# Kernel tuning notes

Hardware: AMD Instinct MI355X
Metric: run time of the kernel (lower is better)

## Reference

```python
import jax, jax.numpy as jnp
import numpy as np

B, S, DIM, H = 2, 4096, 512, 8
HD = DIM // H
SCALE = HD ** -0.5
EPS = 1e-5


def setup_inputs() -> dict:
    key = jax.random.key(0)
    ks = jax.random.split(key, 7)
    std = DIM ** -0.5
    return {
        "x": jax.random.normal(ks[0], (B, S, DIM), dtype=jnp.float32),
        "ln_gamma": jnp.ones((DIM,), jnp.float32),
        "ln_beta": jnp.zeros((DIM,), jnp.float32),
        "w_q": jax.random.normal(ks[1], (DIM, DIM), jnp.float32) * std,
        "w_k": jax.random.normal(ks[2], (DIM, DIM), jnp.float32) * std,
        "w_v": jax.random.normal(ks[3], (DIM, DIM), jnp.float32) * std,
        "w_fc": jax.random.normal(ks[4], (DIM, DIM), jnp.float32) * std,
    }


def reference(x, ln_gamma, ln_beta, w_q, w_k, w_v, w_fc):
    # LayerNorm over last dim
    mu = jnp.mean(x, axis=-1, keepdims=True)
    var = jnp.var(x, axis=-1, keepdims=True)
    xn = (x - mu) * jax.lax.rsqrt(var + EPS) * ln_gamma + ln_beta
    # QKV projections (torch Linear: y = x @ W.T), split into heads -> [B,H,S,HD]
    q = jnp.einsum('bsd,ed->bse', xn, w_q).reshape(B, S, H, HD).transpose(0, 2, 1, 3)
    k = jnp.einsum('bsd,ed->bse', xn, w_k).reshape(B, S, H, HD).transpose(0, 2, 1, 3)
    v = jnp.einsum('bsd,ed->bse', xn, w_v).reshape(B, S, H, HD).transpose(0, 2, 1, 3)
    # scores [B,H,S,S]
    attn = jnp.einsum('bhqd,bhkd->bhqk', q, k) * SCALE
    attn = jax.nn.softmax(attn, axis=-1)
    # dropout is identity in eval mode
    out = jnp.einsum('bhqk,bhkd->bhqd', attn, v)
    out = out.transpose(0, 2, 1, 3).reshape(B, S, DIM)
    return jnp.einsum('bsd,ed->bse', out, w_fc)
```

## Files before the change

### kernel.cpp

```cpp
#include <hip/hip_runtime.h>
#include <cstdint>
#include <cstddef>

typedef unsigned short u16;
typedef unsigned int   u32;
typedef __bf16 bf16x8 __attribute__((ext_vector_type(8)));
typedef float  f32x4  __attribute__((ext_vector_type(4)));
typedef float  f32x16 __attribute__((ext_vector_type(16)));
typedef u16    u16x8  __attribute__((ext_vector_type(8)));
typedef u16    u16x4  __attribute__((ext_vector_type(4)));
typedef u32    u32x2  __attribute__((ext_vector_type(2)));
typedef u32    u32x4  __attribute__((ext_vector_type(4)));

#define DI __device__ __forceinline__

constexpr int SEQ = 4096;
constexpr int DIM = 512;
constexpr int NH  = 8;
constexpr int HD  = 64;
constexpr float ATT_C1 = 0.125f * 1.44269504088896340736f;

DI u16 f2bf(float f) {
  u32 u = __builtin_bit_cast(u32, f);
  u += 0x7fffu + ((u >> 16) & 1u);
  return (u16)(u >> 16);
}

DI u32 pk2(float hi, float lo) {
  u32 uh = __builtin_bit_cast(u32, hi) + 0x8000u;
  u32 ul = __builtin_bit_cast(u32, lo) + 0x8000u;
  return __builtin_amdgcn_perm(uh, ul, 0x07060302u);
}

__global__ __launch_bounds__(256) void wconv_kernel(
    const float* __restrict__ wq, const float* __restrict__ wk,
    const float* __restrict__ wv, const float* __restrict__ wfc,
    u16* __restrict__ Wb)
{
  const int idx  = blockIdx.x * 256 + threadIdx.x;
  const int base = idx * 8;
  const int mat  = base >> 18;
  const int off  = base & (512 * 512 - 1);
  const float* src = (mat == 0) ? wq : (mat == 1) ? wk : (mat == 2) ? wv : wfc;
  const float4 a = *(const float4*)(src + off);
  const float4 b = *(const float4*)(src + off + 4);
  u32x4 o = { pk2(a.y, a.x), pk2(a.w, a.z), pk2(b.y, b.x), pk2(b.w, b.z) };
  *(u32x4*)(Wb + base) = o;
}

__global__ __launch_bounds__(256) void ln_cast_kernel(
    const float* __restrict__ x, const float* __restrict__ gamma,
    const float* __restrict__ beta, u16* __restrict__ xn)
{
  const int row  = blockIdx.x * 4 + (threadIdx.x >> 6);
  const int lane = threadIdx.x & 63;
  const float* xr = x + (size_t)row * DIM + lane * 8;
  const float4 a = *(const float4*)xr;
  const float4 b = *(const float4*)(xr + 4);
  float s = a.x + a.y + a.z + a.w + b.x + b.y + b.z + b.w;
  float q = a.x*a.x + a.y*a.y + a.z*a.z + a.w*a.w
          + b.x*b.x + b.y*b.y + b.z*b.z + b.w*b.w;
#pragma unroll
  for (int m = 1; m < 64; m <<= 1) {
    s += __shfl_xor(s, m, 64);
    q += __shfl_xor(q, m, 64);
  }
  const float mu = s * (1.0f / DIM);
  const float rs = rsqrtf(q * (1.0f / DIM) - mu * mu + 1e-5f);
  const float4 g0 = *(const float4*)(gamma + lane * 8);
  const float4 g1 = *(const float4*)(gamma + lane * 8 + 4);
  const float4 e0 = *(const float4*)(beta + lane * 8);
  const float4 e1 = *(const float4*)(beta + lane * 8 + 4);
  const float v0 = (a.x - mu) * rs * g0.x + e0.x;
  const float v1 = (a.y - mu) * rs * g0.y + e0.y;
  const float v2 = (a.z - mu) * rs * g0.z + e0.z;
  const float v3 = (a.w - mu) * rs * g0.w + e0.w;
  const float v4 = (b.x - mu) * rs * g1.x + e1.x;
  const float v5 = (b.y - mu) * rs * g1.y + e1.y;
  const float v6 = (b.z - mu) * rs * g1.z + e1.z;
  const float v7 = (b.w - mu) * rs * g1.w + e1.w;
  u32x4 o = { pk2(v1, v0), pk2(v3, v2), pk2(v5, v4), pk2(v7, v6) };
  *(u32x4*)(xn + (size_t)row * DIM + lane * 8) = o;
}

template<int MODE>
__global__ __launch_bounds__(256, 2) void gemm_kernel(
    const u16* __restrict__ A, const u16* __restrict__ Wb,
    u16* __restrict__ Qo, u16* __restrict__ Ko, u16* __restrict__ Vt,
    float* __restrict__ Co)
{
  __shared__ u16 As[128][72];
  __shared__ u16 Bs[128][72];
  const int m0 = blockIdx.y * 128, n0 = blockIdx.x * 128;
  const int t = threadIdx.x, wave = t >> 6, lane = t & 63;
  const int quad = lane >> 4, l15 = lane & 15;
  const int wm = wave >> 1, wn = wave & 1;
  const u16* Wsrc;
  if (MODE == 0) {
    const int mat = n0 >> 9;
    Wsrc = Wb + (size_t)mat * 512 * 512 + (size_t)(n0 & 511) * DIM;
  } else {
    Wsrc = Wb + (size_t)3 * 512 * 512 + (size_t)n0 * DIM;
  }

  f32x4 acc[4][4];
#pragma unroll
  for (int i = 0; i < 4; i++)
#pragma unroll
    for (int j = 0; j < 4; j++)
#pragma unroll
      for (int r = 0; r < 4; r++) acc[i][j][r] = 0.0f;

  for (int kk = 0; kk < DIM; kk += 64) {
    __syncthreads();
#pragma unroll
    for (int it = 0; it < 4; it++) {
      const int c4 = t + it * 256;
      const int r = c4 >> 3, off = (c4 & 7) * 8;
      *(u16x8*)&As[r][off] =
          *(const u16x8*)(A + (size_t)(m0 + r) * DIM + kk + off);
      *(u16x8*)&Bs[r][off] =
          *(const u16x8*)(Wsrc + (size_t)r * DIM + kk + off);
    }
    __syncthreads();
#pragma unroll
    for (int kx = 0; kx < 2; kx++) {
      bf16x8 af[4], bfr[4];
#pragma unroll
      for (int i = 0; i < 4; i++)
        af[i] = *(const bf16x8*)&As[wm * 64 + i * 16 + l15][kx * 32 + quad * 8];
#pragma unroll
      for (int j = 0; j < 4; j++)
        bfr[j] = *(const bf16x8*)&Bs[wn * 64 + j * 16 + l15][kx * 32 + quad * 8];
#pragma unroll
      for (int i = 0; i < 4; i++)
#pragma unroll
        for (int j = 0; j < 4; j++)
          acc[i][j] = __builtin_amdgcn_mfma_f32_16x16x32_bf16(
              af[i], bfr[j], acc[i][j], 0, 0, 0);
    }
  }

  if (MODE == 1) {
#pragma unroll
    for (int i = 0; i < 4; i++) {
      const int m = m0 + wm * 64 + i * 16 + quad * 4;
#pragma unroll
      for (int j = 0; j < 4; j++) {
        const int n = n0 + wn * 64 + j * 16 + l15;
#pragma unroll
        for (int r = 0; r < 4; r++)
          Co[(size_t)(m + r) * DIM + n] = acc[i][j][r];
      }
    }
  } else {
    const int mat = n0 >> 9;
    const float qs = (mat == 0) ? ATT_C1 : 1.0f;
#pragma unroll
    for (int i = 0; i < 4; i++) {
      const int m = m0 + wm * 64 + i * 16 + quad * 4;
      const int b = m >> 12, s = m & 4095;
#pragma unroll
      for (int j = 0; j < 4; j++) {
        const int ng = (n0 & 511) + wn * 64 + j * 16 + l15;
        const int h = ng >> 6, d = ng & 63;
        if (mat < 2) {
          u16* dst = (mat == 0 ? Qo : Ko) +
                     ((size_t)(b * NH + h) * SEQ) * HD + d;
#pragma unroll
          for (int r = 0; r < 4; r++)
            dst[(size_t)(s + r) * HD] = f2bf(acc[i][j][r] * qs);
        } else {
          u32x2 w;
          w[0] = pk2(acc[i][j][1], acc[i][j][0]);
          w[1] = pk2(acc[i][j][3], acc[i][j][2]);
          *(u32x2*)&Vt[((size_t)(b * NH + h) * HD + d) * SEQ + s] = w;
        }
      }
    }
  }
}

__global__ __launch_bounds__(256, 2) void attn_kernel(
    const u16* __restrict__ Q, const u16* __restrict__ K,
    const u16* __restrict__ Vt, u16* __restrict__ O)
{
  __shared__ u16 Kl[128][72];
  __shared__ u16 Vl[64][136];
  __shared__ u16 Pl[4][32][136];
  const int qt = blockIdx.x, bh = blockIdx.y;
  const int b = bh >> 3, h = bh & 7;
  const int t = threadIdx.x, wave = t >> 6, lane = t & 63;
  const int l31 = lane & 31, hf = lane >> 5;
  const u16* Qb = Q + (size_t)bh * SEQ * HD;
  const u16* Kb = K + (size_t)bh * SEQ * HD;
  const u16* Vb = Vt + (size_t)bh * HD * SEQ;
  const int qw = qt * 128 + wave * 32;

  bf16x8 bq[4];
#pragma unroll
  for (int kk = 0; kk < 4; kk++)
    bq[kk] = *(const bf16x8*)(Qb + (size_t)(qw + l31) * HD + kk * 16 + hf * 8);

  f32x16 oacc[2];
#pragma unroll
  for (int mt = 0; mt < 2; mt++)
#pragma unroll
    for (int r = 0; r < 16; r++) oacc[mt][r] = 0.0f;
  float lrun = 0.0f;

  for (int kc = 0; kc < SEQ; kc += 128) {
    __syncthreads();
#pragma unroll
    for (int it = 0; it < 4; it++) {
      const int c4 = t + it * 256;
      {
        const int r = c4 >> 3, off = (c4 & 7) * 8;
        *(u16x8*)&Kl[r][off] =
            *(const u16x8*)(Kb + (size_t)(kc + r) * HD + off);
      }
      {
        const int d = c4 >> 4, off = (c4 & 15) * 8;
        *(u16x8*)&Vl[d][off] =
            *(const u16x8*)(Vb + (size_t)d * SEQ + kc + off);
      }
    }
    __syncthreads();

    f32x16 sacc[4];
#pragma unroll
    for (int mt = 0; mt < 4; mt++)
#pragma unroll
      for (int r = 0; r < 16; r++) sacc[mt][r] = 0.0f;
#pragma unroll
    for (int kk = 0; kk < 4; kk++) {
#pragma unroll
      for (int mt = 0; mt < 4; mt++) {
        const bf16x8 ka =
            *(const bf16x8*)&Kl[mt * 32 + l31][kk * 16 + hf * 8];
        sacc[mt] = __builtin_amdgcn_mfma_f32_32x32x16_bf16(
            ka, bq[kk], sacc[mt], 0, 0, 0);
      }
    }

    float ps = 0.0f;
#pragma unroll
    for (int mt = 0; mt < 4; mt++)
#pragma unroll
      for (int r = 0; r < 16; r++) {
        const float p = __builtin_amdgcn_exp2f(sacc[mt][r]);
        sacc[mt][r] = p;
        ps += p;
      }
    lrun += ps;

#pragma unroll
    for (int mt = 0; mt < 4; mt++)
#pragma unroll
      for (int g = 0; g < 4; g++) {
        u32x2 w;
        w[0] = pk2(sacc[mt][g * 4 + 1], sacc[mt][g * 4 + 0]);
        w[1] = pk2(sacc[mt][g * 4 + 3], sacc[mt][g * 4 + 2]);
        *(u32x2*)&Pl[wave][l31][mt * 32 + g * 8 + hf * 4] = w;
      }

#pragma unroll
    for (int kk2 = 0; kk2 < 8; kk2++) {
      const bf16x8 pb = *(const bf16x8*)&Pl[wave][l31][kk2 * 16 + hf * 8];
#pragma unroll
      for (int mt2 = 0; mt2 < 2; mt2++) {
        const bf16x8 va =
            *(const bf16x8*)&Vl[mt2 * 32 + l31][kk2 * 16 + hf * 8];
        oacc[mt2] = __builtin_amdgcn_mfma_f32_32x32x16_bf16(
            va, pb, oacc[mt2], 0, 0, 0);
      }
    }
  }

  const float lt = lrun + __shfl_xor(lrun, 32, 64);
  const float inv = 1.0f / lt;
  const int s = qw + l31;
  u16* Ob = O + ((size_t)(b * SEQ + s)) * DIM + h * HD;
#pragma unroll
  for (int mt2 = 0; mt2 < 2; mt2++)
#pragma unroll
    for (int g = 0; g < 4; g++) {
      u32x2 w;
      w[0] = pk2(oacc[mt2][g * 4 + 1] * inv, oacc[mt2][g * 4 + 0] * inv);
      w[1] = pk2(oacc[mt2][g * 4 + 3] * inv, oacc[mt2][g * 4 + 2] * inv);
      *(u32x2*)&Ob[mt2 * 32 + g * 8 + hf * 4] = w;
    }
}

extern "C" void kernel_launch(void* const* d_in, const int* in_sizes, int n_in,
                              void* d_out, int out_size, void* d_ws,
                              size_t ws_size, hipStream_t stream)
{
  const float* x     = (const float*)d_in[0];
  const float* gamma = (const float*)d_in[1];
  const float* beta  = (const float*)d_in[2];
  const float* wq    = (const float*)d_in[3];
  const float* wk    = (const float*)d_in[4];
  const float* wv    = (const float*)d_in[5];
  const float* wfc   = (const float*)d_in[6];
  float* out = (float*)d_out;

  char* ws = (char*)d_ws;
  u16* xn = (u16*)(ws);
  u16* Qb = (u16*)(ws + ((size_t)8  << 20));
  u16* Kb = (u16*)(ws + ((size_t)16 << 20));
  u16* Vt = (u16*)(ws + ((size_t)24 << 20));
  u16* Ob = (u16*)(ws + ((size_t)32 << 20));
  u16* Wb = (u16*)(ws + ((size_t)40 << 20));

  wconv_kernel<<<512, 256, 0, stream>>>(wq, wk, wv, wfc, Wb);
  ln_cast_kernel<<<2048, 256, 0, stream>>>(x, gamma, beta, xn);
  gemm_kernel<0><<<dim3(12, 64), 256, 0, stream>>>(xn, Wb, Qb, Kb, Vt, nullptr);
  attn_kernel<<<dim3(32, 16), 256, 0, stream>>>(Qb, Kb, Vt, Ob);
  gemm_kernel<1><<<dim3(4, 64), 256, 0, stream>>>(
      Ob, Wb, nullptr, nullptr, nullptr, out);
}
```

Measured before the change: 214.4 us.

## Keep P in registers via permlane swap, prefetch K/V to registers, remap blocks

The attention kernel no longer round-trips the softmax probabilities through LDS. It packs them with v_cvt_pk_bf16_f32 and rearranges them with v_permlane32_swap into the MFMA B-operand layout. Next-tile K/V loads are issued into registers before compute to overlap global latency, and QK^T, exp and PV are interleaved per 32-key subtile with s_setprio hints. Block indices are also remapped to interleave heads across CUs. This relies on gfx950-specific instructions and on the permlane swap exactly matching the MFMA layout, and it adds register pressure.

```diff
diff --git a/kernel.cpp b/kernel.cpp
--- a/kernel.cpp
+++ b/kernel.cpp
@@ -30,6 +30,16 @@
   u32 uh = __builtin_bit_cast(u32, hi) + 0x8000u;
   u32 ul = __builtin_bit_cast(u32, lo) + 0x8000u;
   return __builtin_amdgcn_perm(uh, ul, 0x07060302u);
+}
+
+DI u32 cvtpk(float a, float b) {
+  u32 r;
+  asm("v_cvt_pk_bf16_f32 %0, %1, %2" : "=v"(r) : "v"(a), "v"(b));
+  return r;
+}
+
+DI void plswap(u32& a, u32& b) {
+  asm("v_permlane32_swap_b32 %0, %1" : "+v"(a), "+v"(b));
 }
 
 __global__ __launch_bounds__(256) void wconv_kernel(
@@ -187,8 +197,10 @@
 {
   __shared__ u16 Kl[128][72];
   __shared__ u16 Vl[64][136];
-  __shared__ u16 Pl[4][32][136];
-  const int qt = blockIdx.x, bh = blockIdx.y;
+  const int flat = blockIdx.x + 32 * blockIdx.y;
+  const int slot = flat >> 3;
+  const int bh = (flat & 7) * 2 + (slot & 1);
+  const int qt = slot >> 1;
   const int b = bh >> 3, h = bh & 7;
   const int t = threadIdx.x, wave = t >> 6, lane = t & 63;
   const int l31 = lane & 31, hf = lane >> 5;
@@ -209,71 +221,87 @@
     for (int r = 0; r < 16; r++) oacc[mt][r] = 0.0f;
   float lrun = 0.0f;
 
+  const int st_r  = t >> 3,  st_off = (t & 7) * 8;
+  const int st_d  = t >> 4,  st_o2  = (t & 15) * 8;
+
+  u16x8 kst[4], vst[4];
+#pragma unroll
+  for (int it = 0; it < 4; it++) {
+    const int c4 = t + it * 256;
+    const int r = c4 >> 3, off = (c4 & 7) * 8;
+    kst[it] = *(const u16x8*)(Kb + (size_t)r * HD + off);
+    const int d = c4 >> 4, o2 = (c4 & 15) * 8;
+    vst[it] = *(const u16x8*)(Vb + (size_t)d * SEQ + o2);
+  }
+
   for (int kc = 0; kc < SEQ; kc += 128) {
     __syncthreads();
 #pragma unroll
     for (int it = 0; it < 4; it++) {
       const int c4 = t + it * 256;
-      {
+      const int r = c4 >> 3, off = (c4 & 7) * 8;
+      *(u16x8*)&Kl[r][off] = kst[it];
+      const int d = c4 >> 4, o2 = (c4 & 15) * 8;
+      *(u16x8*)&Vl[d][o2] = vst[it];
+    }
+    __syncthreads();
+    if (kc + 128 < SEQ) {
+#pragma unroll
+      for (int it = 0; it < 4; it++) {
+        const int c4 = t + it * 256;
         const int r = c4 >> 3, off = (c4 & 7) * 8;
-        *(u16x8*)&Kl[r][off] =
-            *(const u16x8*)(Kb + (size_t)(kc + r) * HD + off);
-      }
-      {
-        const int d = c4 >> 4, off = (c4 & 15) * 8;
-        *(u16x8*)&Vl[d][off] =
-            *(const u16x8*)(Vb + (size_t)d * SEQ + kc + off);
-      }
-    }
-    __syncthreads();
-
-    f32x16 sacc[4];
-#pragma unroll
-    for (int mt = 0; mt < 4; mt++)
-#pragma unroll
-      for (int r = 0; r < 16; r++) sacc[mt][r] = 0.0f;
-#pragma unroll
-    for (int kk = 0; kk < 4; kk++) {
-#pragma unroll
-      for (int mt = 0; mt < 4; mt++) {
+        kst[it] = *(const u16x8*)(Kb + (size_t)(kc + 128 + r) * HD + off);
+        const int d = c4 >> 4, o2 = (c4 & 15) * 8;
+        vst[it] = *(const u16x8*)(Vb + (size_t)d * SEQ + kc + 128 + o2);
+      }
+    }
+
+#pragma unroll
+    for (int mt = 0; mt < 4; mt++) {
+      f32x16 s;
+#pragma unroll
+      for (int r = 0; r < 16; r++) s[r] = 0.0f;
+      __builtin_amdgcn_s_setprio(1);
+#pragma unroll
+      for (int kk = 0; kk < 4; kk++) {
         const bf16x8 ka =
             *(const bf16x8*)&Kl[mt * 32 + l31][kk * 16 + hf * 8];
-        sacc[mt] = __builtin_amdgcn_mfma_f32_32x32x16_bf16(
-            ka, bq[kk], sacc[mt], 0, 0, 0);
-      }
-    }
-
-    float ps = 0.0f;
-#pragma unroll
-    for (int mt = 0; mt < 4; mt++)
-#pragma unroll
-      for (int r = 0; r < 16; r++) {
-        const float p = __builtin_amdgcn_exp2f(sacc[mt][r]);
-        sacc[mt][r] = p;
-        ps += p;
-      }
-    lrun += ps;
-
-#pragma unroll
-    for (int mt = 0; mt < 4; mt++)
-#pragma unroll
-      for (int g = 0; g < 4; g++) {
-        u32x2 w;
-        w[0] = pk2(sacc[mt][g * 4 + 1], sacc[mt][g * 4 + 0]);
-        w[1] = pk2(sacc[mt][g * 4 + 3], sacc[mt][g * 4 + 2]);
-        *(u32x2*)&Pl[wave][l31][mt * 32 + g * 8 + hf * 4] = w;
-      }
-
-#pragma unroll
-    for (int kk2 = 0; kk2 < 8; kk2++) {
-      const bf16x8 pb = *(const bf16x8*)&Pl[wave][l31][kk2 * 16 + hf * 8];
+        s = __builtin_amdgcn_mfma_f32_32x32x16_bf16(ka, bq[kk], s, 0, 0, 0);
+      }
+      __builtin_amdgcn_s_setprio(0);
+
+      float e[16];
+#pragma unroll
+      for (int r = 0; r < 16; r++) e[r] = __builtin_amdgcn_exp2f(s[r]);
+      lrun += (((e[0] + e[1]) + (e[2] + e[3])) +
+               ((e[4] + e[5]) + (e[6] + e[7]))) +
+              (((e[8] + e[9]) + (e[10] + e[11])) +
+               ((e[12] + e[13]) + (e[14] + e[15])));
+
+      u32 a0 = cvtpk(e[0],  e[1]),  a1 = cvtpk(e[2],  e[3]);
+      u32 a2 = cvtpk(e[4],  e[5]),  a3 = cvtpk(e[6],  e[7]);
+      plswap(a0, a2); plswap(a1, a3);
+      u32 c0 = cvtpk(e[8],  e[9]),  c1 = cvtpk(e[10], e[11]);
+      u32 c2 = cvtpk(e[12], e[13]), c3 = cvtpk(e[14], e[15]);
+      plswap(c0, c2); plswap(c1, c3);
+      u32x4 f0v = { a0, a1, a2, a3 };
+      u32x4 f1v = { c0, c1, c2, c3 };
+      const bf16x8 p0 = __builtin_bit_cast(bf16x8, f0v);
+      const bf16x8 p1 = __builtin_bit_cast(bf16x8, f1v);
+
+      __builtin_amdgcn_s_setprio(1);
 #pragma unroll
       for (int mt2 = 0; mt2 < 2; mt2++) {
-        const bf16x8 va =
-            *(const bf16x8*)&Vl[mt2 * 32 + l31][kk2 * 16 + hf * 8];
+        const bf16x8 va0 =
+            *(const bf16x8*)&Vl[mt2 * 32 + l31][(mt * 2 + 0) * 16 + hf * 8];
         oacc[mt2] = __builtin_amdgcn_mfma_f32_32x32x16_bf16(
-            va, pb, oacc[mt2], 0, 0, 0);
-      }
+            va0, p0, oacc[mt2], 0, 0, 0);
+        const bf16x8 va1 =
+            *(const bf16x8*)&Vl[mt2 * 32 + l31][(mt * 2 + 1) * 16 + hf * 8];
+        oacc[mt2] = __builtin_amdgcn_mfma_f32_32x32x16_bf16(
+            va1, p1, oacc[mt2], 0, 0, 0);
+      }
+      __builtin_amdgcn_s_setprio(0);
     }
   }
 
```

Result: faster. 200.4 us (-6.5%).
